# Kernel tuning notes

Measured on AMD Instinct MI355X. Metric: run time of the kernel, lower is better.

## Reference

```python
import jax, jax.numpy as jnp
import numpy as np

NUM_HEADS = 12
DIM = 768
HEAD_DIM = DIM // NUM_HEADS
NUM_BUCKETS = 32
MAX_DISTANCE = 128
ELEV_SCALE = 1000.0


def _bucket_positions(relative_position):
    # Faithful port of RelativePositionBias2D._bucket_positions (torch .long() truncates;
    # values passed through the large branch are non-negative so astype(int32) matches).
    nb = NUM_BUCKETS // 2  # 16
    n = -relative_position
    ret = (n < 0).astype(jnp.int32) * nb
    n = jnp.abs(n)
    max_exact = nb // 2  # 8
    is_small = n < max_exact
    n_safe = jnp.maximum(n, 1).astype(jnp.float32)  # avoid log(0); masked by is_small
    val_if_large = max_exact + (
        jnp.log(n_safe / max_exact) / np.float32(np.log(MAX_DISTANCE / max_exact)) * (nb - max_exact)
    ).astype(jnp.int32)
    val_if_large = jnp.minimum(val_if_large, nb - 1)
    return ret + jnp.where(is_small, n, val_if_large)


def _bucket_idx(coords_2d):
    # coords_2d: [B, N, 2] in [0,1] -> integer grid coords
    coords_int = (coords_2d * MAX_DISTANCE).astype(jnp.int32)
    rel_x = coords_int[:, :, None, 0] - coords_int[:, None, :, 0]  # [B,N,N]
    rel_y = coords_int[:, :, None, 1] - coords_int[:, None, :, 1]
    bx = _bucket_positions(rel_x)
    by = _bucket_positions(rel_y)
    return bx * NUM_BUCKETS + by  # [B,N,N] int32 in [0, 1024)


def setup_inputs() -> dict:
    key = jax.random.key(0)
    ks = jax.random.split(key, 8)
    B, N, D = 4, 1024, DIM
    x = jax.random.normal(ks[0], (B, N, D), dtype=jnp.float32)
    coords_2d = jax.random.uniform(ks[1], (B, N, 2), dtype=jnp.float32)
    elevation_patches = jax.random.normal(ks[2], (B, N), dtype=jnp.float32) * 2000.0  # meters
    qkv_w = jax.random.normal(ks[3], (3 * D, D), dtype=jnp.float32) * 0.02
    qkv_b = jnp.zeros((3 * D,), dtype=jnp.float32)
    proj_w = jax.random.normal(ks[4], (D, D), dtype=jnp.float32) * 0.02
    proj_b = jnp.zeros((D,), dtype=jnp.float32)
    bias_table = jax.random.normal(ks[5], (NUM_BUCKETS * NUM_BUCKETS, NUM_HEADS), dtype=jnp.float32) * 0.02
    alpha = jnp.full((1,), 2.0, dtype=jnp.float32)
    return {"x": x, "coords_2d": coords_2d, "elevation_patches": elevation_patches,
            "qkv_w": qkv_w, "qkv_b": qkv_b, "proj_w": proj_w, "proj_b": proj_b,
            "bias_table": bias_table, "alpha": alpha}


def reference(x, coords_2d, elevation_patches, qkv_w, qkv_b, proj_w, proj_b, bias_table, alpha):
    B, N, D = x.shape
    H, hd = NUM_HEADS, HEAD_DIM
    scale = hd ** -0.5

    qkv = x @ qkv_w.T + qkv_b  # [B,N,3D]
    qkv = qkv.reshape(B, N, 3, H, hd)
    q = qkv[:, :, 0].transpose(0, 2, 1, 3)  # [B,H,N,hd]
    k = qkv[:, :, 1].transpose(0, 2, 1, 3)
    v = qkv[:, :, 2].transpose(0, 2, 1, 3)

    attn = jnp.einsum('bhnd,bhmd->bhnm', q * scale, k)  # [B,H,N,N]

    # relative position bias: gather from table, [B,N,N,H] -> [B,H,N,N]
    idx = _bucket_idx(coords_2d)
    rel_bias = bias_table[idx].transpose(0, 3, 1, 2)
    attn = attn + rel_bias

    # elevation bias: [B,N,N], broadcast over heads
    elev_diff = (elevation_patches[:, None, :] - elevation_patches[:, :, None]) / ELEV_SCALE
    elev_bias = jnp.clip(-alpha[0] * jax.nn.relu(elev_diff), -10.0, 0.0)
    attn = attn + elev_bias[:, None, :, :]

    attn = jax.nn.softmax(attn.astype(jnp.float32), axis=-1).astype(q.dtype)

    out = jnp.einsum('bhnm,bhmd->bhnd', attn, v)  # [B,H,N,hd]
    out = out.transpose(0, 2, 1, 3).reshape(B, N, D)
    return out @ proj_w.T + proj_b
```

## Files before the change

### kernel.cpp

```cpp
#include <hip/hip_runtime.h>
#include <hip/hip_bf16.h>
#include <math.h>

#define NH 12
#define HD 64
#define NSEQ 1024
#define DMODEL 768
#define LOG2E 1.44269504f

typedef unsigned short ushort_t;
typedef float f32x4 __attribute__((ext_vector_type(4)));
typedef short bf16x8 __attribute__((ext_vector_type(8)));

__device__ __forceinline__ ushort_t f2bf(float f) {
    unsigned int u = __float_as_uint(f);
    u += 0x7FFFu + ((u >> 16) & 1u);
    return (ushort_t)(u >> 16);
}

__device__ __forceinline__ unsigned pk2(float x, float y) {
    __hip_bfloat162 t = __float22bfloat162_rn(make_float2(x, y));
    union { __hip_bfloat162 b; unsigned u; } c; c.b = t;
    return c.u;
}

__device__ __forceinline__ void gl_lds16(const ushort_t* g, ushort_t* l) {
    __builtin_amdgcn_global_load_lds(
        (const __attribute__((address_space(1))) unsigned int*)g,
        (__attribute__((address_space(3))) unsigned int*)l, 16, 0, 0);
}

#define XB_N   3145728u
#define WQB_N  1769472u
#define PWB_N  589824u
#define CVT_BLOCKS 2688

__global__ __launch_bounds__(256) void prep_kernel(
    const float* __restrict__ x, const float* __restrict__ w1,
    const float* __restrict__ w2, ushort_t* __restrict__ dst)
{
    const int t = threadIdx.x;
    const unsigned i = blockIdx.x * 256 + t;
    const unsigned n0 = XB_N / 8, n1 = n0 + WQB_N / 8, n2 = n1 + PWB_N / 8;
    if (i >= n2) return;
    const float* src; unsigned off;
    if (i < n0)      { src = x;  off = i; }
    else if (i < n1) { src = w1; off = i - n0; }
    else             { src = w2; off = i - n1; }
    const float4 a = ((const float4*)src)[off * 2];
    const float4 b = ((const float4*)src)[off * 2 + 1];
    uint4 pk;
    pk.x = pk2(a.x, a.y); pk.y = pk2(a.z, a.w);
    pk.z = pk2(b.x, b.y); pk.w = pk2(b.z, b.w);
    ((uint4*)dst)[i] = pk;
}

__device__ __forceinline__ int bucketf(int rel) {
    const int n = -rel;
    const int u = (n < 0) ? 16 : 0;
    const int a = n < 0 ? -n : n;
    if (a < 8) return u + a;
    int v = 8 + (int)(log2f((float)a * 0.125f) * 2.0f + 1e-4f);
    if (v > 15) v = 15;
    return u + v;
}

#define QKV_BLOCKS 576

__global__ __launch_bounds__(256) void qkv_gemm(
    const ushort_t* __restrict__ A, const ushort_t* __restrict__ B,
    const float* __restrict__ bias,
    ushort_t* __restrict__ Qb, ushort_t* __restrict__ Kb, ushort_t* __restrict__ Vtb,
    const float* __restrict__ coords, const float* __restrict__ elev,
    const float* __restrict__ alpha_p, unsigned* __restrict__ pack)
{
    __shared__ __align__(16) ushort_t SM[9216];
    const int t = threadIdx.x;

    if (blockIdx.x >= QKV_BLOCKS) {
        const int blk = blockIdx.x - QKV_BLOCKS;
        const int b = blk >> 10, i = blk & 1023;
        const float alpha = alpha_p[0];
        const float2 ci = *(const float2*)&coords[(size_t)(b * NSEQ + i) * 2];
        const int cxi = (int)(ci.x * 128.0f), cyi = (int)(ci.y * 128.0f);
        const float ei = elev[b * NSEQ + i];
        const int j0 = t * 4;
        const float4 c01 = *(const float4*)&coords[(size_t)(b * NSEQ + j0) * 2];
        const float4 c23 = *(const float4*)&coords[(size_t)(b * NSEQ + j0 + 2) * 2];
        const float4 ej4 = *(const float4*)&elev[b * NSEQ + j0];
        const float cjx[4] = {c01.x, c01.z, c23.x, c23.z};
        const float cjy[4] = {c01.y, c01.w, c23.y, c23.w};
        const float ejv[4] = {ej4.x, ej4.y, ej4.z, ej4.w};
        unsigned r[4];
        #pragma unroll
        for (int k = 0; k < 4; ++k) {
            const int bx = bucketf(cxi - (int)(cjx[k] * 128.0f));
            const int by = bucketf(cyi - (int)(cjy[k] * 128.0f));
            const int idx = (bx << 5) + by;
            const float ed = (ejv[k] - ei) * 1e-3f;
            const float eb = fmaxf(-alpha * fmaxf(ed, 0.0f), -10.0f) * LOG2E;
            r[k] = ((unsigned)f2bf(eb) << 16) | (unsigned)idx;
        }
        uint4 o; o.x = r[0]; o.y = r[1]; o.z = r[2]; o.w = r[3];
        *(uint4*)&pack[((size_t)b << 20) + (size_t)i * NSEQ + j0] = o;
        return;
    }

    const int lid = (blockIdx.x & 7) * 72 + (blockIdx.x >> 3);
    const int bx = lid % 18, by = lid / 18;
    const int m0 = by * 128, c0 = bx * 128;

    ushort_t* Asb = SM;
    ushort_t* Bsb = SM + 4096;
    const int lane = t & 63, w = t >> 6;
    const int wr = w >> 1, wc = w & 1;
    const int col = lane & 15, quad = lane >> 4;

    const f32x4 zero = {0.f, 0.f, 0.f, 0.f};
    f32x4 acc[4][4];
    #pragma unroll
    for (int i = 0; i < 4; ++i)
        #pragma unroll
        for (int j = 0; j < 4; ++j) acc[i][j] = zero;

    const int arow = w * 32 + (lane >> 2);
    const int scol = (lane & 3) * 8;
    const ushort_t* Ag = A + (size_t)(m0 + arow) * DMODEL + scol;
    const ushort_t* Bg = B + (size_t)(c0 + arow) * DMODEL + scol;
    ushort_t* Asw = Asb + w * 32 * 32;
    ushort_t* Bsw = Bsb + w * 32 * 32;

    for (int k0 = 0; k0 < DMODEL; k0 += 32) {
        __syncthreads();
        gl_lds16(Ag + k0, Asw);
        gl_lds16(Ag + (size_t)16 * DMODEL + k0, Asw + 16 * 32);
        gl_lds16(Bg + k0, Bsw);
        gl_lds16(Bg + (size_t)16 * DMODEL + k0, Bsw + 16 * 32);
        __syncthreads();
        bf16x8 af[4], bf[4];
        #pragma unroll
        for (int im = 0; im < 4; ++im)
            af[im] = *(const bf16x8*)&Asb[(wr * 64 + im * 16 + col) * 32 + quad * 8];
        #pragma unroll
        for (int jn = 0; jn < 4; ++jn)
            bf[jn] = *(const bf16x8*)&Bsb[(wc * 64 + jn * 16 + col) * 32 + quad * 8];
        #pragma unroll
        for (int im = 0; im < 4; ++im)
            #pragma unroll
            for (int jn = 0; jn < 4; ++jn)
                acc[im][jn] = __builtin_amdgcn_mfma_f32_16x16x32_bf16(af[im], bf[jn], acc[im][jn], 0, 0, 0);
    }

    const int cbw = c0 + wc * 64;
    const int s = cbw / DMODEL;
    const int h = (cbw % DMODEL) >> 6;
    const int b = m0 >> 10;
    const int bh = b * NH + h;
    const int n0 = (m0 & (NSEQ - 1)) + wr * 64;

    float bv[4];
    #pragma unroll
    for (int jn = 0; jn < 4; ++jn) bv[jn] = bias[cbw + jn * 16 + col];

    __syncthreads();

    if (s < 2) {
        ushort_t* lt = SM + w * 1152;
        ushort_t* dst = (s == 0) ? Qb : Kb;
        const float sc = (s == 0) ? 0.125f * LOG2E : 1.0f;
        const int row16 = lane >> 2, seg = lane & 3;
        #pragma unroll
        for (int im = 0; im < 4; ++im) {
            #pragma unroll
            for (int jn = 0; jn < 4; ++jn) {
                const f32x4 a = acc[im][jn];
                #pragma unroll
                for (int r = 0; r < 4; ++r)
                    lt[(quad * 4 + r) * 72 + jn * 16 + col] = f2bf((a[r] + bv[jn]) * sc);
            }
            const uint4 u0 = *(const uint4*)&lt[row16 * 72 + seg * 8];
            const uint4 u1 = *(const uint4*)&lt[row16 * 72 + 32 + seg * 8];
            const size_t gb = ((size_t)bh * NSEQ + n0 + im * 16 + row16) * HD
                            + seg * 8;
            *(uint4*)&dst[gb] = u0;
            *(uint4*)&dst[gb + 32] = u1;
        }
    } else {
        #pragma unroll
        for (int im = 0; im < 4; ++im) {
            #pragma unroll
            for (int jn = 0; jn < 4; ++jn) {
                const int d = jn * 16 + col;
                const float bvv = bv[jn];
                const f32x4 a = acc[im][jn];
                uint2 p;
                p.x = pk2(a[0] + bvv, a[1] + bvv);
                p.y = pk2(a[2] + bvv, a[3] + bvv);
                *(uint2*)&Vtb[((size_t)bh * HD + d) * NSEQ + n0 + im * 16 + quad * 4] = p;
            }
        }
    }
}

#define RBIAS(u) (__uint_as_float((unsigned)tabu[(u) & 1023u] << 16) \
                + __uint_as_float((u) & 0xFFFF0000u))

__global__ __launch_bounds__(256) void attn_mfma(
    const ushort_t* __restrict__ Qb, const ushort_t* __restrict__ Kb,
    const ushort_t* __restrict__ Vtb,
    const unsigned* __restrict__ pack,
    const float* __restrict__ table,
    ushort_t* __restrict__ Ob)
{
    __shared__ __align__(16) ushort_t Ks[2][64 * 72];
    __shared__ __align__(16) ushort_t Vt[2][64 * 72];
    __shared__ __align__(16) ushort_t Ps[64 * 72];
    __shared__ ushort_t tabu[1024];

    const int t = threadIdx.x;
    const int lane = t & 63, w = t >> 6;
    const int col = lane & 15, quad = lane >> 4;
    const int bid = (blockIdx.x & 7) * 96 + (blockIdx.x >> 3);
    const int it = bid & 15, bh = bid >> 4;
    const int h = bh % NH, b = bh / NH;
    const int i0 = it * 64;

    for (int i = t; i < 1024; i += 256)
        tabu[i] = f2bf(table[i * NH + h] * LOG2E);

    const ushort_t* Qg = Qb + ((size_t)bh * NSEQ + i0 + w * 16 + col) * HD;
    const bf16x8 aq0 = *(const bf16x8*)(Qg + quad * 8);
    const bf16x8 aq1 = *(const bf16x8*)(Qg + 32 + quad * 8);

    const size_t kvbase = (size_t)bh * NSEQ * HD;
    const unsigned* prow = pack + ((size_t)b << 20)
                         + (size_t)(i0 + w * 16 + col) * NSEQ + quad * 4;

    const int srow = t >> 3, sc8 = (t & 7) * 8;
    const int so0 = srow * 72 + sc8;
    const int so1 = (srow + 32) * 72 + sc8;

    uint4 k0 = *(const uint4*)&Kb[kvbase + (size_t)srow * HD + sc8];
    uint4 k1 = *(const uint4*)&Kb[kvbase + (size_t)(srow + 32) * HD + sc8];
    uint4 v0 = *(const uint4*)&Vtb[kvbase + (size_t)srow * NSEQ + sc8];
    uint4 v1 = *(const uint4*)&Vtb[kvbase + (size_t)(srow + 32) * NSEQ + sc8];
    *(uint4*)&Ks[0][so0] = k0;
    *(uint4*)&Ks[0][so1] = k1;
    *(uint4*)&Vt[0][so0] = v0;
    *(uint4*)&Vt[0][so1] = v1;
    k0 = *(const uint4*)&Kb[kvbase + (size_t)(64 + srow) * HD + sc8];
    k1 = *(const uint4*)&Kb[kvbase + (size_t)(64 + srow + 32) * HD + sc8];
    v0 = *(const uint4*)&Vtb[kvbase + (size_t)srow * NSEQ + 64 + sc8];
    v1 = *(const uint4*)&Vtb[kvbase + (size_t)(srow + 32) * NSEQ + 64 + sc8];

    uint4 pk4g[4], pk4l[4];
    #pragma unroll
    for (int jb = 0; jb < 4; ++jb)
        pk4g[jb] = *(const uint4*)(prow + jb * 16);

    __syncthreads();

    float rbc[4][4], rbn[4][4];
    #pragma unroll
    for (int jb = 0; jb < 4; ++jb) {
        const uint4 pkv = pk4g[jb];
        rbc[jb][0] = RBIAS(pkv.x);
        rbc[jb][1] = RBIAS(pkv.y);
        rbc[jb][2] = RBIAS(pkv.z);
        rbc[jb][3] = RBIAS(pkv.w);
    }
    #pragma unroll
    for (int jb = 0; jb < 4; ++jb)
        pk4g[jb] = *(const uint4*)(prow + 64 + jb * 16);

    const f32x4 zero = {0.f, 0.f, 0.f, 0.f};
    f32x4 o_acc[4];
    #pragma unroll
    for (int i = 0; i < 4; ++i) o_acc[i] = zero;
    float l_l = 0.f;

    #pragma unroll 2
    for (int jt = 0; jt < 16; ++jt) {
        __syncthreads();
        const int cur = jt & 1;

        if (jt < 15) {
            *(uint4*)&Ks[cur ^ 1][so0] = k0;
            *(uint4*)&Ks[cur ^ 1][so1] = k1;
            *(uint4*)&Vt[cur ^ 1][so0] = v0;
            *(uint4*)&Vt[cur ^ 1][so1] = v1;
        }
        if (jt < 14) {
            const int j2 = (jt + 2) * 64;
            k0 = *(const uint4*)&Kb[kvbase + (size_t)(j2 + srow) * HD + sc8];
            k1 = *(const uint4*)&Kb[kvbase + (size_t)(j2 + srow + 32) * HD + sc8];
            v0 = *(const uint4*)&Vtb[kvbase + (size_t)srow * NSEQ + j2 + sc8];
            v1 = *(const uint4*)&Vtb[kvbase + (size_t)(srow + 32) * NSEQ + j2 + sc8];
            #pragma unroll
            for (int jb = 0; jb < 4; ++jb)
                pk4l[jb] = *(const uint4*)(prow + j2 + jb * 16);
        }

        f32x4 sacc[4];
        __builtin_amdgcn_s_setprio(1);
        #pragma unroll
        for (int jb = 0; jb < 4; ++jb) {
            sacc[jb] = zero;
            const bf16x8 kb0 = *(const bf16x8*)&Ks[cur][(jb * 16 + col) * 72 + quad * 8];
            const bf16x8 kb1 = *(const bf16x8*)&Ks[cur][(jb * 16 + col) * 72 + 32 + quad * 8];
            sacc[jb] = __builtin_amdgcn_mfma_f32_16x16x32_bf16(kb0, aq0, sacc[jb], 0, 0, 0);
            sacc[jb] = __builtin_amdgcn_mfma_f32_16x16x32_bf16(kb1, aq1, sacc[jb], 0, 0, 0);
        }
        __builtin_amdgcn_s_setprio(0);

        float psum = 0.f;
        #pragma unroll
        for (int jb = 0; jb < 4; ++jb) {
            const float p0 = exp2f(sacc[jb][0] + rbc[jb][0]);
            const float p1 = exp2f(sacc[jb][1] + rbc[jb][1]);
            const float p2 = exp2f(sacc[jb][2] + rbc[jb][2]);
            const float p3 = exp2f(sacc[jb][3] + rbc[jb][3]);
            psum += (p0 + p1) + (p2 + p3);
            uint2 st;
            st.x = pk2(p0, p1);
            st.y = pk2(p2, p3);
            *(uint2*)&Ps[(w * 16 + col) * 72 + jb * 16 + quad * 4] = st;
        }
        l_l += psum;

        const bf16x8 ap0 = *(const bf16x8*)&Ps[(w * 16 + col) * 72 + quad * 8];
        const bf16x8 ap1 = *(const bf16x8*)&Ps[(w * 16 + col) * 72 + 32 + quad * 8];
        __builtin_amdgcn_s_setprio(1);
        #pragma unroll
        for (int db = 0; db < 4; ++db) {
            const bf16x8 vv0 = *(const bf16x8*)&Vt[cur][(db * 16 + col) * 72 + quad * 8];
            const bf16x8 vv1 = *(const bf16x8*)&Vt[cur][(db * 16 + col) * 72 + 32 + quad * 8];
            o_acc[db] = __builtin_amdgcn_mfma_f32_16x16x32_bf16(ap0, vv0, o_acc[db], 0, 0, 0);
            o_acc[db] = __builtin_amdgcn_mfma_f32_16x16x32_bf16(ap1, vv1, o_acc[db], 0, 0, 0);
            if (jt < 15) {
                const uint4 pkv = pk4g[db];
                rbn[db][0] = RBIAS(pkv.x);
                rbn[db][1] = RBIAS(pkv.y);
                rbn[db][2] = RBIAS(pkv.z);
                rbn[db][3] = RBIAS(pkv.w);
            }
        }
        __builtin_amdgcn_s_setprio(0);

        #pragma unroll
        for (int jb = 0; jb < 4; ++jb) {
            pk4g[jb] = pk4l[jb];
            rbc[jb][0] = rbn[jb][0];
            rbc[jb][1] = rbn[jb][1];
            rbc[jb][2] = rbn[jb][2];
            rbc[jb][3] = rbn[jb][3];
        }
    }

    float l = l_l;
    l += __shfl_xor(l, 16);
    l += __shfl_xor(l, 32);
    #pragma unroll
    for (int r = 0; r < 4; ++r) {
        const float lr = __shfl(l, w * 16 + quad * 4 + r);
        const float inv = 1.f / lr;
        const int ri = w * 16 + quad * 4 + r;
        const size_t base = ((size_t)(b * NSEQ) + i0 + ri) * DMODEL + h * HD;
        #pragma unroll
        for (int db = 0; db < 4; ++db)
            Ob[base + db * 16 + col] = f2bf(o_acc[db][r] * inv);
    }
}

__global__ __launch_bounds__(256) void proj_gemm(
    const ushort_t* __restrict__ A, const ushort_t* __restrict__ B,
    const float* __restrict__ bias, float* __restrict__ out)
{
    __shared__ __align__(16) ushort_t As[64 * 32];
    __shared__ __align__(16) ushort_t Bs[64 * 32];
    const int t = threadIdx.x;
    const int lane = t & 63, w = t >> 6;
    const int wr = w >> 1, wc = w & 1;
    const int col = lane & 15, quad = lane >> 4;
    const int m0 = blockIdx.y * 64, c0 = blockIdx.x * 64;

    const f32x4 zero = {0.f, 0.f, 0.f, 0.f};
    f32x4 acc[2][2];
    #pragma unroll
    for (int i = 0; i < 2; ++i)
        #pragma unroll
        for (int j = 0; j < 2; ++j) acc[i][j] = zero;

    const int srow = w * 16 + (lane >> 2);
    const int scol = (lane & 3) * 8;
    const ushort_t* Ag = A + (size_t)(m0 + srow) * DMODEL + scol;
    const ushort_t* Bg = B + (size_t)(c0 + srow) * DMODEL + scol;
    ushort_t* Asw = &As[w * 16 * 32];
    ushort_t* Bsw = &Bs[w * 16 * 32];

    for (int k0 = 0; k0 < DMODEL; k0 += 32) {
        __syncthreads();
        gl_lds16(Ag + k0, Asw);
        gl_lds16(Bg + k0, Bsw);
        __syncthreads();
        bf16x8 af[2], bf[2];
        #pragma unroll
        for (int im = 0; im < 2; ++im)
            af[im] = *(const bf16x8*)&As[(wr * 32 + im * 16 + col) * 32 + quad * 8];
        #pragma unroll
        for (int jn = 0; jn < 2; ++jn)
            bf[jn] = *(const bf16x8*)&Bs[(wc * 32 + jn * 16 + col) * 32 + quad * 8];
        #pragma unroll
        for (int im = 0; im < 2; ++im)
            #pragma unroll
            for (int jn = 0; jn < 2; ++jn)
                acc[im][jn] = __builtin_amdgcn_mfma_f32_16x16x32_bf16(af[im], bf[jn], acc[im][jn], 0, 0, 0);
    }

    #pragma unroll
    for (int im = 0; im < 2; ++im) {
        #pragma unroll
        for (int jn = 0; jn < 2; ++jn) {
            const int c = c0 + wc * 32 + jn * 16 + col;
            const float bv = bias[c];
            #pragma unroll
            for (int r = 0; r < 4; ++r) {
                const int m = m0 + wr * 32 + im * 16 + quad * 4 + r;
                out[(size_t)m * DMODEL + c] = acc[im][jn][r] + bv;
            }
        }
    }
}

extern "C" void kernel_launch(void* const* d_in, const int* in_sizes, int n_in,
                              void* d_out, int out_size, void* d_ws, size_t ws_size,
                              hipStream_t stream) {
    const float* x       = (const float*)d_in[0];
    const float* coords  = (const float*)d_in[1];
    const float* elev    = (const float*)d_in[2];
    const float* qkv_w   = (const float*)d_in[3];
    const float* qkv_b   = (const float*)d_in[4];
    const float* proj_w  = (const float*)d_in[5];
    const float* proj_b  = (const float*)d_in[6];
    const float* btable  = (const float*)d_in[7];
    const float* alpha   = (const float*)d_in[8];
    float* out = (float*)d_out;

    ushort_t* wsu = (ushort_t*)d_ws;
    ushort_t* xb  = wsu;
    ushort_t* wqb = wsu + 3145728;
    ushort_t* pwb = wsu + 4915200;
    ushort_t* Qb  = wsu + 5505024;
    ushort_t* Kb  = wsu + 8650752;
    ushort_t* Vtb = wsu + 11796480;
    ushort_t* Ob  = wsu + 14942208;
    unsigned* pck = (unsigned*)(wsu + 18087936);

    prep_kernel<<<CVT_BLOCKS, 256, 0, stream>>>(x, qkv_w, proj_w, wsu);
    qkv_gemm<<<QKV_BLOCKS + 4096, 256, 0, stream>>>(
        xb, wqb, qkv_b, Qb, Kb, Vtb, coords, elev, alpha, pck);
    attn_mfma<<<768, 256, 0, stream>>>(Qb, Kb, Vtb, pck, btable, Ob);
    proj_gemm<<<dim3(12, 64), 256, 0, stream>>>(Ob, pwb, proj_b, out);
}
```

Measured before the change: 182.7 us.

## Double GEMM K-step to 64 with XOR-swizzled LDS and move proj_w conversion

Both the QKV and projection GEMMs now stage 64-wide K slices per barrier pair instead of 32. The slices go into LDS with an XOR swizzle on 16-byte groups to avoid bank conflicts on the fragment reads. This halves the number of __syncthreads iterations, at the cost of twice the shared memory per block. The proj_w fp32-to-bf16 conversion moves out of the prep kernel into extra blocks of the QKV GEMM launch, so it overlaps with GEMM work and the prep kernel gets smaller.

Result: faster. 170.1 us (-6.9%).

```diff
diff --git a/kernel.cpp b/kernel.cpp
--- a/kernel.cpp
+++ b/kernel.cpp
@@ -33,20 +33,19 @@
 #define XB_N   3145728u
 #define WQB_N  1769472u
 #define PWB_N  589824u
-#define CVT_BLOCKS 2688
+#define CVT_BLOCKS 2400
 
 __global__ __launch_bounds__(256) void prep_kernel(
     const float* __restrict__ x, const float* __restrict__ w1,
-    const float* __restrict__ w2, ushort_t* __restrict__ dst)
+    ushort_t* __restrict__ dst)
 {
     const int t = threadIdx.x;
     const unsigned i = blockIdx.x * 256 + t;
-    const unsigned n0 = XB_N / 8, n1 = n0 + WQB_N / 8, n2 = n1 + PWB_N / 8;
-    if (i >= n2) return;
+    const unsigned n0 = XB_N / 8, n1 = n0 + WQB_N / 8;
+    if (i >= n1) return;
     const float* src; unsigned off;
-    if (i < n0)      { src = x;  off = i; }
-    else if (i < n1) { src = w1; off = i - n0; }
-    else             { src = w2; off = i - n1; }
+    if (i < n0) { src = x;  off = i; }
+    else        { src = w1; off = i - n0; }
     const float4 a = ((const float4*)src)[off * 2];
     const float4 b = ((const float4*)src)[off * 2 + 1];
     uint4 pk;
@@ -66,17 +65,31 @@
 }
 
 #define QKV_BLOCKS 576
+#define PACK_BLOCKS 4096
+#define PW_BLOCKS 288
 
 __global__ __launch_bounds__(256) void qkv_gemm(
     const ushort_t* __restrict__ A, const ushort_t* __restrict__ B,
     const float* __restrict__ bias,
     ushort_t* __restrict__ Qb, ushort_t* __restrict__ Kb, ushort_t* __restrict__ Vtb,
     const float* __restrict__ coords, const float* __restrict__ elev,
-    const float* __restrict__ alpha_p, unsigned* __restrict__ pack)
+    const float* __restrict__ alpha_p, unsigned* __restrict__ pack,
+    const float* __restrict__ pw, ushort_t* __restrict__ pwb)
 {
-    __shared__ __align__(16) ushort_t SM[9216];
+    __shared__ __align__(16) ushort_t SM[16384];
     const int t = threadIdx.x;
 
+    if (blockIdx.x >= QKV_BLOCKS + PACK_BLOCKS) {
+        const unsigned i = (blockIdx.x - QKV_BLOCKS - PACK_BLOCKS) * 256 + t;
+        if (i >= PWB_N / 8) return;
+        const float4 a = ((const float4*)pw)[i * 2];
+        const float4 b = ((const float4*)pw)[i * 2 + 1];
+        uint4 pk;
+        pk.x = pk2(a.x, a.y); pk.y = pk2(a.z, a.w);
+        pk.z = pk2(b.x, b.y); pk.w = pk2(b.z, b.w);
+        ((uint4*)pwb)[i] = pk;
+        return;
+    }
     if (blockIdx.x >= QKV_BLOCKS) {
         const int blk = blockIdx.x - QKV_BLOCKS;
         const int b = blk >> 10, i = blk & 1023;
@@ -111,10 +124,11 @@
     const int m0 = by * 128, c0 = bx * 128;
 
     ushort_t* Asb = SM;
-    ushort_t* Bsb = SM + 4096;
+    ushort_t* Bsb = SM + 8192;
     const int lane = t & 63, w = t >> 6;
     const int wr = w >> 1, wc = w & 1;
     const int col = lane & 15, quad = lane >> 4;
+    const int c7 = col & 7;
 
     const f32x4 zero = {0.f, 0.f, 0.f, 0.f};
     f32x4 acc[4][4];
@@ -123,32 +137,41 @@
         #pragma unroll
         for (int j = 0; j < 4; ++j) acc[i][j] = zero;
 
-    const int arow = w * 32 + (lane >> 2);
-    const int scol = (lane & 3) * 8;
-    const ushort_t* Ag = A + (size_t)(m0 + arow) * DMODEL + scol;
-    const ushort_t* Bg = B + (size_t)(c0 + arow) * DMODEL + scol;
-    ushort_t* Asw = Asb + w * 32 * 32;
-    ushort_t* Bsw = Bsb + w * 32 * 32;
-
-    for (int k0 = 0; k0 < DMODEL; k0 += 32) {
+    const int r8 = lane >> 3, g8 = lane & 7;
+    const int gsw = ((g8 ^ r8) * 8);
+    const ushort_t* Ag = A + (size_t)(m0 + w * 32 + r8) * DMODEL + gsw;
+    const ushort_t* Bg = B + (size_t)(c0 + w * 32 + r8) * DMODEL + gsw;
+    ushort_t* Asw = Asb + (w * 32) * 64;
+    ushort_t* Bsw = Bsb + (w * 32) * 64;
+
+    for (int k0 = 0; k0 < DMODEL; k0 += 64) {
         __syncthreads();
         gl_lds16(Ag + k0, Asw);
-        gl_lds16(Ag + (size_t)16 * DMODEL + k0, Asw + 16 * 32);
+        gl_lds16(Ag + (size_t)8 * DMODEL + k0, Asw + 8 * 64);
+        gl_lds16(Ag + (size_t)16 * DMODEL + k0, Asw + 16 * 64);
+        gl_lds16(Ag + (size_t)24 * DMODEL + k0, Asw + 24 * 64);
         gl_lds16(Bg + k0, Bsw);
-        gl_lds16(Bg + (size_t)16 * DMODEL + k0, Bsw + 16 * 32);
+        gl_lds16(Bg + (size_t)8 * DMODEL + k0, Bsw + 8 * 64);
+        gl_lds16(Bg + (size_t)16 * DMODEL + k0, Bsw + 16 * 64);
+        gl_lds16(Bg + (size_t)24 * DMODEL + k0, Bsw + 24 * 64);
         __syncthreads();
-        bf16x8 af[4], bf[4];
-        #pragma unroll
-        for (int im = 0; im < 4; ++im)
-            af[im] = *(const bf16x8*)&Asb[(wr * 64 + im * 16 + col) * 32 + quad * 8];
-        #pragma unroll
-        for (int jn = 0; jn < 4; ++jn)
-            bf[jn] = *(const bf16x8*)&Bsb[(wc * 64 + jn * 16 + col) * 32 + quad * 8];
-        #pragma unroll
-        for (int im = 0; im < 4; ++im)
+        #pragma unroll
+        for (int kk = 0; kk < 2; ++kk) {
+            bf16x8 af[4], bf[4];
+            #pragma unroll
+            for (int im = 0; im < 4; ++im)
+                af[im] = *(const bf16x8*)&Asb[(wr * 64 + im * 16 + col) * 64
+                        + ((4 * kk + quad) ^ c7) * 8];
             #pragma unroll
             for (int jn = 0; jn < 4; ++jn)
-                acc[im][jn] = __builtin_amdgcn_mfma_f32_16x16x32_bf16(af[im], bf[jn], acc[im][jn], 0, 0, 0);
+                bf[jn] = *(const bf16x8*)&Bsb[(wc * 64 + jn * 16 + col) * 64
+                        + ((4 * kk + quad) ^ c7) * 8];
+            #pragma unroll
+            for (int im = 0; im < 4; ++im)
+                #pragma unroll
+                for (int jn = 0; jn < 4; ++jn)
+                    acc[im][jn] = __builtin_amdgcn_mfma_f32_16x16x32_bf16(af[im], bf[jn], acc[im][jn], 0, 0, 0);
+        }
     }
 
     const int cbw = c0 + wc * 64;
@@ -376,12 +399,13 @@
     const ushort_t* __restrict__ A, const ushort_t* __restrict__ B,
     const float* __restrict__ bias, float* __restrict__ out)
 {
-    __shared__ __align__(16) ushort_t As[64 * 32];
-    __shared__ __align__(16) ushort_t Bs[64 * 32];
+    __shared__ __align__(16) ushort_t As[64 * 64];
+    __shared__ __align__(16) ushort_t Bs[64 * 64];
     const int t = threadIdx.x;
     const int lane = t & 63, w = t >> 6;
     const int wr = w >> 1, wc = w & 1;
     const int col = lane & 15, quad = lane >> 4;
+    const int c7 = col & 7;
     const int m0 = blockIdx.y * 64, c0 = blockIdx.x * 64;
 
     const f32x4 zero = {0.f, 0.f, 0.f, 0.f};
@@ -391,30 +415,37 @@
         #pragma unroll
         for (int j = 0; j < 2; ++j) acc[i][j] = zero;
 
-    const int srow = w * 16 + (lane >> 2);
-    const int scol = (lane & 3) * 8;
-    const ushort_t* Ag = A + (size_t)(m0 + srow) * DMODEL + scol;
-    const ushort_t* Bg = B + (size_t)(c0 + srow) * DMODEL + scol;
-    ushort_t* Asw = &As[w * 16 * 32];
-    ushort_t* Bsw = &Bs[w * 16 * 32];
-
-    for (int k0 = 0; k0 < DMODEL; k0 += 32) {
+    const int r8 = lane >> 3, g8 = lane & 7;
+    const int gsw = ((g8 ^ r8) * 8);
+    const ushort_t* Ag = A + (size_t)(m0 + w * 16 + r8) * DMODEL + gsw;
+    const ushort_t* Bg = B + (size_t)(c0 + w * 16 + r8) * DMODEL + gsw;
+    ushort_t* Asw = &As[(w * 16) * 64];
+    ushort_t* Bsw = &Bs[(w * 16) * 64];
+
+    for (int k0 = 0; k0 < DMODEL; k0 += 64) {
         __syncthreads();
         gl_lds16(Ag + k0, Asw);
+        gl_lds16(Ag + (size_t)8 * DMODEL + k0, Asw + 8 * 64);
         gl_lds16(Bg + k0, Bsw);
+        gl_lds16(Bg + (size_t)8 * DMODEL + k0, Bsw + 8 * 64);
         __syncthreads();
-        bf16x8 af[2], bf[2];
-        #pragma unroll
-        for (int im = 0; im < 2; ++im)
-            af[im] = *(const bf16x8*)&As[(wr * 32 + im * 16 + col) * 32 + quad * 8];
-        #pragma unroll
-        for (int jn = 0; jn < 2; ++jn)
-            bf[jn] = *(const bf16x8*)&Bs[(wc * 32 + jn * 16 + col) * 32 + quad * 8];
-        #pragma unroll
-        for (int im = 0; im < 2; ++im)
+        #pragma unroll
+        for (int kk = 0; kk < 2; ++kk) {
+            bf16x8 af[2], bf[2];
+            #pragma unroll
+            for (int im = 0; im < 2; ++im)
+                af[im] = *(const bf16x8*)&As[(wr * 32 + im * 16 + col) * 64
+                        + ((4 * kk + quad) ^ c7) * 8];
             #pragma unroll
             for (int jn = 0; jn < 2; ++jn)
-                acc[im][jn] = __builtin_amdgcn_mfma_f32_16x16x32_bf16(af[im], bf[jn], acc[im][jn], 0, 0, 0);
+                bf[jn] = *(const bf16x8*)&Bs[(wc * 32 + jn * 16 + col) * 64
+                        + ((4 * kk + quad) ^ c7) * 8];
+            #pragma unroll
+            for (int im = 0; im < 2; ++im)
+                #pragma unroll
+                for (int jn = 0; jn < 2; ++jn)
+                    acc[im][jn] = __builtin_amdgcn_mfma_f32_16x16x32_bf16(af[im], bf[jn], acc[im][jn], 0, 0, 0);
+        }
     }
 
     #pragma unroll
@@ -456,9 +487,9 @@
     ushort_t* Ob  = wsu + 14942208;
     unsigned* pck = (unsigned*)(wsu + 18087936);
 
-    prep_kernel<<<CVT_BLOCKS, 256, 0, stream>>>(x, qkv_w, proj_w, wsu);
-    qkv_gemm<<<QKV_BLOCKS + 4096, 256, 0, stream>>>(
-        xb, wqb, qkv_b, Qb, Kb, Vtb, coords, elev, alpha, pck);
+    prep_kernel<<<CVT_BLOCKS, 256, 0, stream>>>(x, qkv_w, wsu);
+    qkv_gemm<<<QKV_BLOCKS + PACK_BLOCKS + PW_BLOCKS, 256, 0, stream>>>(
+        xb, wqb, qkv_b, Qb, Kb, Vtb, coords, elev, alpha, pck, proj_w, pwb);
     attn_mfma<<<768, 256, 0, stream>>>(Qb, Kb, Vtb, pck, btable, Ob);
     proj_gemm<<<dim3(12, 64), 256, 0, stream>>>(Ob, pwb, proj_b, out);
 }
```
